# Kernel tuning notes

Hardware: AMD Instinct MI355X
Metric: run time of the kernel (lower is better)

The kernel has to match this reference:

```python
import jax, jax.numpy as jnp
import numpy as np

B, N, D, P = 4, 16384, 128, 100


def setup_inputs() -> dict:
    key = jax.random.key(0)
    k1, k2, k3 = jax.random.split(key, 3)
    x = jax.random.normal(k1, (B, N, D), dtype=jnp.float32)
    y = jax.random.normal(k2, (B, N, D), dtype=jnp.float32)
    thetas = jax.random.normal(k3, (P, D), dtype=jnp.float32)
    return {"x": x, "y": y, "thetas": thetas}


def reference(x, y, thetas):
    # Sliced OT (the branch taken since B*N*N*4 bytes >> memory limit).
    n_proj = thetas.shape[0]
    # F.normalize(theta, dim=0) per projection direction (eps clamp 1e-12)
    norms = jnp.maximum(jnp.linalg.norm(thetas, axis=-1, keepdims=True), 1e-12)
    thetas = thetas / norms  # (P, d)

    # Project all points onto all directions: (P, B, N)
    x_proj = jnp.einsum('bnd,pd->pbn', x, thetas)
    y_proj = jnp.einsum('bnd,pd->pbn', y, thetas)

    # torch: sort y_proj; scatter y_sorted back to original order of x via
    # x_indices = argsort(x_proj). Equivalent: transported_proj[n] =
    # y_sorted[rank_of_x_proj[n]], with rank = argsort(argsort(.)).
    y_sorted = jnp.sort(y_proj, axis=-1)
    ranks = jnp.argsort(jnp.argsort(x_proj, axis=-1), axis=-1)
    transported_proj = jnp.take_along_axis(y_sorted, ranks, axis=-1)  # (P, B, N)

    # Accumulate (transported_proj - x_proj) * theta over projections.
    transported = jnp.einsum('pbn,pd->bnd', transported_proj - x_proj, thetas)
    return x + transported / n_proj
```

## Files before the change

kernel.cpp:

```cpp
#include <hip/hip_runtime.h>
#include <hip/hip_bf16.h>

#define B_    4
#define N_    16384
#define D_    128
#define P_    100
#define BN_   65536
#define PBN_  6553600
#define PPAD  112
#define KPAD  128
#define NBIN  4096

typedef __attribute__((ext_vector_type(8))) short short8;
typedef __attribute__((ext_vector_type(4))) float floatx4;

__device__ __forceinline__ unsigned short f2b(float f) {
    unsigned u = __float_as_uint(f);
    return (unsigned short)((u + 0x7FFFu + ((u >> 16) & 1u)) >> 16);
}
__device__ __forceinline__ float b2f(unsigned short h) {
    return __uint_as_float(((unsigned)h) << 16);
}

__global__ void k_norm(const float* __restrict__ th,
                       unsigned short* __restrict__ thb,
                       unsigned short* __restrict__ thbT) {
    int p = blockIdx.x;
    int d = threadIdx.x;
    float v = 0.f;
    if (p < P_) v = th[p * D_ + d];
    float s = v * v;
    #pragma unroll
    for (int o = 32; o > 0; o >>= 1) s += __shfl_down(s, o, 64);
    __shared__ float red[2];
    if ((d & 63) == 0) red[d >> 6] = s;
    __syncthreads();
    float norm = fmaxf(sqrtf(red[0] + red[1]), 1e-12f);
    unsigned short r = f2b(v / norm);
    if (p < PPAD) thb[p * D_ + d] = r;
    thbT[d * KPAD + p] = r;
}

__global__ __launch_bounds__(256, 4) void k_proj(
    const float* __restrict__ x, const float* __restrict__ y,
    const unsigned short* __restrict__ thb,
    unsigned short* __restrict__ xp, unsigned short* __restrict__ yp) {
    __shared__ unsigned short th_s[15232];
    __shared__ unsigned short buf[8064];
    const int tid  = threadIdx.x;
    const int w    = tid >> 6;
    const int lane = tid & 63;
    const int n    = lane & 15;
    const int quad = lane >> 4;
    const int row0 = blockIdx.x * 64;

    for (int g = tid; g < 1792; g += 256) {
        int r = g >> 4, c = (g & 15) << 3;
        *(uint4*)(th_s + r * 136 + c) = *(const uint4*)(thb + r * D_ + c);
    }

    const float* xr = x + (size_t)(row0 + w * 16 + n) * D_ + quad * 8;
    const float* yr = y + (size_t)(row0 + w * 16 + n) * D_ + quad * 8;
    short8 bx[4], by[4];
    {
        float4 lx[8];
        #pragma unroll
        for (int ks = 0; ks < 4; ++ks) {
            lx[2*ks]   = *(const float4*)(xr + ks * 32);
            lx[2*ks+1] = *(const float4*)(xr + ks * 32 + 4);
        }
        #pragma unroll
        for (int ks = 0; ks < 4; ++ks) {
            short8 t;
            t[0] = (short)f2b(lx[2*ks].x);   t[1] = (short)f2b(lx[2*ks].y);
            t[2] = (short)f2b(lx[2*ks].z);   t[3] = (short)f2b(lx[2*ks].w);
            t[4] = (short)f2b(lx[2*ks+1].x); t[5] = (short)f2b(lx[2*ks+1].y);
            t[6] = (short)f2b(lx[2*ks+1].z); t[7] = (short)f2b(lx[2*ks+1].w);
            bx[ks] = t;
        }
    }
    {
        float4 ly[8];
        #pragma unroll
        for (int ks = 0; ks < 4; ++ks) {
            ly[2*ks]   = *(const float4*)(yr + ks * 32);
            ly[2*ks+1] = *(const float4*)(yr + ks * 32 + 4);
        }
        #pragma unroll
        for (int ks = 0; ks < 4; ++ks) {
            short8 t;
            t[0] = (short)f2b(ly[2*ks].x);   t[1] = (short)f2b(ly[2*ks].y);
            t[2] = (short)f2b(ly[2*ks].z);   t[3] = (short)f2b(ly[2*ks].w);
            t[4] = (short)f2b(ly[2*ks+1].x); t[5] = (short)f2b(ly[2*ks+1].y);
            t[6] = (short)f2b(ly[2*ks+1].z); t[7] = (short)f2b(ly[2*ks+1].w);
            by[ks] = t;
        }
    }
    __syncthreads();

    floatx4 ay[7];
    #pragma unroll
    for (int pt = 0; pt < 7; ++pt) {
        floatx4 accx = {0.f, 0.f, 0.f, 0.f};
        floatx4 accy = {0.f, 0.f, 0.f, 0.f};
        #pragma unroll
        for (int ks = 0; ks < 4; ++ks) {
            short8 a = *(const short8*)(th_s + (pt * 16 + n) * 136 + ks * 32 + quad * 8);
            accx = __builtin_amdgcn_mfma_f32_16x16x32_bf16(a, bx[ks], accx, 0, 0, 0);
            accy = __builtin_amdgcn_mfma_f32_16x16x32_bf16(a, by[ks], accy, 0, 0, 0);
        }
        #pragma unroll
        for (int reg = 0; reg < 4; ++reg)
            buf[(pt * 16 + quad * 4 + reg) * 72 + w * 16 + n] = f2b(accx[reg]);
        ay[pt] = accy;
    }
    __syncthreads();

    for (int g = tid; g < 800; g += 256) {
        int p = g >> 3, c = (g & 7) << 3;
        *(uint4*)(xp + (size_t)p * BN_ + row0 + c) = *(const uint4*)(buf + p * 72 + c);
    }
    __syncthreads();

    #pragma unroll
    for (int pt = 0; pt < 7; ++pt)
        #pragma unroll
        for (int reg = 0; reg < 4; ++reg)
            buf[(pt * 16 + quad * 4 + reg) * 72 + w * 16 + n] = f2b(ay[pt][reg]);
    __syncthreads();

    for (int g = tid; g < 800; g += 256) {
        int p = g >> 3, c = (g & 7) << 3;
        *(uint4*)(yp + (size_t)p * BN_ + row0 + c) = *(const uint4*)(buf + p * 72 + c);
    }
}

__device__ __forceinline__ int binof(float v) {
    int k = (int)((v + 8.0f) * 256.0f);
    return k < 0 ? 0 : (k > NBIN - 1 ? NBIN - 1 : k);
}

__device__ __forceinline__ void scan4(unsigned* hist, volatile unsigned* wsum, int t) {
    unsigned v[4], run = 0;
    #pragma unroll
    for (int i = 0; i < 4; ++i) { unsigned h = hist[t * 4 + i]; v[i] = run; run += h; }
    const int lane = t & 63, w = t >> 6;
    unsigned inc = run;
    #pragma unroll
    for (int off = 1; off < 64; off <<= 1) {
        unsigned nbr = __shfl_up(inc, off, 64);
        if (lane >= off) inc += nbr;
    }
    if (lane == 63) wsum[w] = inc;
    __syncthreads();
    if (t == 0) {
        unsigned r2 = 0;
        #pragma unroll
        for (int i = 0; i < 16; ++i) { unsigned h = wsum[i]; wsum[i] = r2; r2 += h; }
    }
    __syncthreads();
    unsigned base = wsum[w] + (inc - run);
    #pragma unroll
    for (int i = 0; i < 4; ++i) hist[t * 4 + i] = base + v[i];
}

__global__ __launch_bounds__(1024, 4) void k_sortdiff(
    const unsigned short* __restrict__ xp, const unsigned short* __restrict__ yp,
    unsigned short* __restrict__ diff) {
    __shared__ unsigned hist[NBIN];
    __shared__ unsigned short ysort[N_];
    __shared__ unsigned wsum[16];
    const int t = threadIdx.x;
    const unsigned* ypd = (const unsigned*)(yp + (size_t)blockIdx.x * N_);
    const unsigned* xpd = (const unsigned*)(xp + (size_t)blockIdx.x * N_);
    unsigned*       dfd = (unsigned*)(diff + (size_t)blockIdx.x * N_);

    unsigned yw[8], xw[8];
    #pragma unroll
    for (int i = 0; i < 2; ++i) {
        uint4 a = *(const uint4*)(ypd + i * 4096 + t * 4);
        yw[4*i] = a.x; yw[4*i+1] = a.y; yw[4*i+2] = a.z; yw[4*i+3] = a.w;
        uint4 c = *(const uint4*)(xpd + i * 4096 + t * 4);
        xw[4*i] = c.x; xw[4*i+1] = c.y; xw[4*i+2] = c.z; xw[4*i+3] = c.w;
    }

    #pragma unroll
    for (int i = 0; i < 4; ++i) hist[t + i * 1024] = 0;
    __syncthreads();

    unsigned jy[8], jx[8];
    #pragma unroll
    for (int k = 0; k < 8; ++k) {
        unsigned j0 = atomicAdd(&hist[binof(b2f((unsigned short)(yw[k] & 0xffff)))], 1u);
        unsigned j1 = atomicAdd(&hist[binof(b2f((unsigned short)(yw[k] >> 16)))], 1u);
        jy[k] = (j0 & 0xffffu) | (j1 << 16);
        unsigned i0 = atomicAdd(&hist[binof(b2f((unsigned short)(xw[k] & 0xffff)))], 0x10000u);
        unsigned i1 = atomicAdd(&hist[binof(b2f((unsigned short)(xw[k] >> 16)))], 0x10000u);
        jx[k] = (i0 >> 16) | (i1 & 0xffff0000u);
    }
    __syncthreads();
    scan4(hist, wsum, t);
    __syncthreads();

    #pragma unroll
    for (int k = 0; k < 8; ++k) {
        unsigned short e0 = (unsigned short)(yw[k] & 0xffff);
        unsigned short e1 = (unsigned short)(yw[k] >> 16);
        ysort[(hist[binof(b2f(e0))] & 0xffffu) + (jy[k] & 0xffffu)] = e0;
        ysort[(hist[binof(b2f(e1))] & 0xffffu) + (jy[k] >> 16)]     = e1;
        unsigned r0 = (hist[binof(b2f((unsigned short)(xw[k] & 0xffff)))] >> 16) + (jx[k] & 0xffffu);
        unsigned r1 = (hist[binof(b2f((unsigned short)(xw[k] >> 16)))] >> 16) + (jx[k] >> 16);
        jx[k] = r0 | (r1 << 16);
    }
    __syncthreads();

    #pragma unroll
    for (int i = 0; i < 2; ++i) {
        unsigned o[4];
        #pragma unroll
        for (int q = 0; q < 4; ++q) {
            int k = 4*i + q;
            float x0 = b2f((unsigned short)(xw[k] & 0xffff));
            float x1 = b2f((unsigned short)(xw[k] >> 16));
            unsigned short d0 = f2b(b2f(ysort[jx[k] & 0xffffu]) - x0);
            unsigned short d1 = f2b(b2f(ysort[jx[k] >> 16]) - x1);
            o[q] = (unsigned)d0 | ((unsigned)d1 << 16);
        }
        *(uint4*)(dfd + i * 4096 + t * 4) = make_uint4(o[0], o[1], o[2], o[3]);
    }
}

__global__ __launch_bounds__(256) void k_comb(
    const float* __restrict__ x, const unsigned short* __restrict__ diff,
    const unsigned short* __restrict__ thbT, float* __restrict__ out) {
    __shared__ unsigned short ths[128 * 136];
    __shared__ unsigned Lp[64 * 68];
    const int tid  = threadIdx.x;
    const int w    = tid >> 6;
    const int lane = tid & 63;
    const int n16  = lane & 15;
    const int quad = lane >> 4;
    const int row0 = blockIdx.x * 64;

    for (int g = tid; g < 2048; g += 256) {
        int r = g >> 4, c = (g & 15) << 3;
        *(uint4*)(ths + r * 136 + c) = *(const uint4*)(thbT + r * KPAD + c);
    }
    for (int g = tid; g < 952; g += 256) Lp[50 * 68 + g] = 0;
    for (int g = tid; g < 400; g += 256) {
        int p2 = g >> 3, rg = (g & 7) << 3;
        uint4 a = *(const uint4*)(diff + (size_t)(2 * p2) * BN_ + row0 + rg);
        uint4 b = *(const uint4*)(diff + (size_t)(2 * p2 + 1) * BN_ + row0 + rg);
        unsigned* dst = Lp + p2 * 68 + rg;
        dst[0] = (a.x & 0xffffu) | (b.x << 16);
        dst[1] = (a.x >> 16)     | (b.x & 0xffff0000u);
        dst[2] = (a.y & 0xffffu) | (b.y << 16);
        dst[3] = (a.y >> 16)     | (b.y & 0xffff0000u);
        dst[4] = (a.z & 0xffffu) | (b.z << 16);
        dst[5] = (a.z >> 16)     | (b.z & 0xffff0000u);
        dst[6] = (a.w & 0xffffu) | (b.w << 16);
        dst[7] = (a.w >> 16)     | (b.w & 0xffff0000u);
    }
    __syncthreads();

    const int r = w * 16 + n16;
    short8 af[4];
    #pragma unroll
    for (int ks = 0; ks < 4; ++ks) {
        union { unsigned u[4]; short8 v; } tu;
        #pragma unroll
        for (int m = 0; m < 4; ++m)
            tu.u[m] = Lp[(ks * 16 + quad * 4 + m) * 68 + r];
        af[ks] = tu.v;
    }

    floatx4 acc[8];
    #pragma unroll
    for (int nt = 0; nt < 8; ++nt) {
        acc[nt] = (floatx4){0.f, 0.f, 0.f, 0.f};
        #pragma unroll
        for (int ks = 0; ks < 4; ++ks) {
            short8 b = *(const short8*)(ths + (nt * 16 + n16) * 136 + ks * 32 + quad * 8);
            acc[nt] = __builtin_amdgcn_mfma_f32_16x16x32_bf16(af[ks], b, acc[nt], 0, 0, 0);
        }
    }

    const float invP = 1.0f / (float)P_;
    const size_t rbase = (size_t)(row0 + w * 16 + quad * 4) * D_ + n16;
    #pragma unroll
    for (int nt = 0; nt < 8; ++nt)
        #pragma unroll
        for (int reg = 0; reg < 4; ++reg) {
            size_t o = rbase + (size_t)reg * D_ + nt * 16;
            out[o] = fmaf(acc[nt][reg], invP, x[o]);
        }
}

extern "C" void kernel_launch(void* const* d_in, const int* in_sizes, int n_in,
                              void* d_out, int out_size, void* d_ws, size_t ws_size,
                              hipStream_t stream) {
    const float* x  = (const float*)d_in[0];
    const float* y  = (const float*)d_in[1];
    const float* th = (const float*)d_in[2];
    float* out = (float*)d_out;
    char*  wsb = (char*)d_ws;

    unsigned short* thb  = (unsigned short*)wsb;
    unsigned short* thbT = (unsigned short*)(wsb + 32768);
    unsigned short* xpb  = (unsigned short*)(wsb + 65536);
    unsigned short* ypb  = xpb + PBN_;

    k_norm<<<128, 128, 0, stream>>>(th, thb, thbT);
    k_proj<<<BN_ / 64, 256, 0, stream>>>(x, y, thb, xpb, ypb);
    k_sortdiff<<<P_ * B_, 1024, 0, stream>>>(xpb, ypb, xpb);
    k_comb<<<BN_ / 64, 256, 0, stream>>>(x, xpb, thbT, out);
}
```

Baseline: 144.2 us.

## Halve LDS staging buffers in projection and combine kernels to raise occupancy

The projection kernel now writes its x/y projection tiles in two passes (rows 0-63, then 64-111) through a smaller LDS buffer, so each block needs less shared memory. The combine kernel stages only half of the transposed theta matrix at a time, reloading the second half after the first half's output is written, and adds launch bounds of 4. The goal is more resident blocks per CU to hide memory latency, at the cost of extra barriers, a second theta load per block, and more serialized store phases.

After: 140.7 us. 1.03x faster.

```diff
diff --git a/kernel.cpp b/kernel.cpp
--- a/kernel.cpp
+++ b/kernel.cpp
@@ -46,7 +46,7 @@
     const unsigned short* __restrict__ thb,
     unsigned short* __restrict__ xp, unsigned short* __restrict__ yp) {
     __shared__ unsigned short th_s[15232];
-    __shared__ unsigned short buf[8064];
+    __shared__ unsigned short buf[4608];
     const int tid  = threadIdx.x;
     const int w    = tid >> 6;
     const int lane = tid & 63;
@@ -99,8 +99,9 @@
     __syncthreads();
 
     floatx4 ay[7];
-    #pragma unroll
-    for (int pt = 0; pt < 7; ++pt) {
+
+    #pragma unroll
+    for (int pt = 0; pt < 4; ++pt) {
         floatx4 accx = {0.f, 0.f, 0.f, 0.f};
         floatx4 accy = {0.f, 0.f, 0.f, 0.f};
         #pragma unroll
@@ -115,23 +116,55 @@
         ay[pt] = accy;
     }
     __syncthreads();
-
-    for (int g = tid; g < 800; g += 256) {
+    for (int g = tid; g < 512; g += 256) {
         int p = g >> 3, c = (g & 7) << 3;
         *(uint4*)(xp + (size_t)p * BN_ + row0 + c) = *(const uint4*)(buf + p * 72 + c);
     }
     __syncthreads();
 
     #pragma unroll
-    for (int pt = 0; pt < 7; ++pt)
+    for (int pt = 4; pt < 7; ++pt) {
+        floatx4 accx = {0.f, 0.f, 0.f, 0.f};
+        floatx4 accy = {0.f, 0.f, 0.f, 0.f};
+        #pragma unroll
+        for (int ks = 0; ks < 4; ++ks) {
+            short8 a = *(const short8*)(th_s + (pt * 16 + n) * 136 + ks * 32 + quad * 8);
+            accx = __builtin_amdgcn_mfma_f32_16x16x32_bf16(a, bx[ks], accx, 0, 0, 0);
+            accy = __builtin_amdgcn_mfma_f32_16x16x32_bf16(a, by[ks], accy, 0, 0, 0);
+        }
+        #pragma unroll
+        for (int reg = 0; reg < 4; ++reg)
+            buf[((pt - 4) * 16 + quad * 4 + reg) * 72 + w * 16 + n] = f2b(accx[reg]);
+        ay[pt] = accy;
+    }
+    __syncthreads();
+    for (int g = tid; g < 288; g += 256) {
+        int p = g >> 3, c = (g & 7) << 3;
+        *(uint4*)(xp + (size_t)(64 + p) * BN_ + row0 + c) = *(const uint4*)(buf + p * 72 + c);
+    }
+    __syncthreads();
+
+    #pragma unroll
+    for (int pt = 0; pt < 4; ++pt)
         #pragma unroll
         for (int reg = 0; reg < 4; ++reg)
             buf[(pt * 16 + quad * 4 + reg) * 72 + w * 16 + n] = f2b(ay[pt][reg]);
     __syncthreads();
-
-    for (int g = tid; g < 800; g += 256) {
+    for (int g = tid; g < 512; g += 256) {
         int p = g >> 3, c = (g & 7) << 3;
         *(uint4*)(yp + (size_t)p * BN_ + row0 + c) = *(const uint4*)(buf + p * 72 + c);
+    }
+    __syncthreads();
+
+    #pragma unroll
+    for (int pt = 4; pt < 7; ++pt)
+        #pragma unroll
+        for (int reg = 0; reg < 4; ++reg)
+            buf[((pt - 4) * 16 + quad * 4 + reg) * 72 + w * 16 + n] = f2b(ay[pt][reg]);
+    __syncthreads();
+    for (int g = tid; g < 288; g += 256) {
+        int p = g >> 3, c = (g & 7) << 3;
+        *(uint4*)(yp + (size_t)(64 + p) * BN_ + row0 + c) = *(const uint4*)(buf + p * 72 + c);
     }
 }
 
@@ -230,10 +263,10 @@
     }
 }
 
-__global__ __launch_bounds__(256) void k_comb(
+__global__ __launch_bounds__(256, 4) void k_comb(
     const float* __restrict__ x, const unsigned short* __restrict__ diff,
     const unsigned short* __restrict__ thbT, float* __restrict__ out) {
-    __shared__ unsigned short ths[128 * 136];
+    __shared__ unsigned short ths[64 * 136];
     __shared__ unsigned Lp[64 * 68];
     const int tid  = threadIdx.x;
     const int w    = tid >> 6;
@@ -242,7 +275,7 @@
     const int quad = lane >> 4;
     const int row0 = blockIdx.x * 64;
 
-    for (int g = tid; g < 2048; g += 256) {
+    for (int g = tid; g < 1024; g += 256) {
         int r = g >> 4, c = (g & 15) << 3;
         *(uint4*)(ths + r * 136 + c) = *(const uint4*)(thbT + r * KPAD + c);
     }
@@ -274,26 +307,45 @@
         af[ks] = tu.v;
     }
 
-    floatx4 acc[8];
-    #pragma unroll
-    for (int nt = 0; nt < 8; ++nt) {
-        acc[nt] = (floatx4){0.f, 0.f, 0.f, 0.f};
-        #pragma unroll
-        for (int ks = 0; ks < 4; ++ks) {
-            short8 b = *(const short8*)(ths + (nt * 16 + n16) * 136 + ks * 32 + quad * 8);
-            acc[nt] = __builtin_amdgcn_mfma_f32_16x16x32_bf16(af[ks], b, acc[nt], 0, 0, 0);
-        }
-    }
-
     const float invP = 1.0f / (float)P_;
     const size_t rbase = (size_t)(row0 + w * 16 + quad * 4) * D_ + n16;
-    #pragma unroll
-    for (int nt = 0; nt < 8; ++nt)
+
+    #pragma unroll
+    for (int nt = 0; nt < 4; ++nt) {
+        floatx4 acc = {0.f, 0.f, 0.f, 0.f};
+        #pragma unroll
+        for (int ks = 0; ks < 4; ++ks) {
+            short8 b = *(const short8*)(ths + (nt * 16 + n16) * 136 + ks * 32 + quad * 8);
+            acc = __builtin_amdgcn_mfma_f32_16x16x32_bf16(af[ks], b, acc, 0, 0, 0);
+        }
         #pragma unroll
         for (int reg = 0; reg < 4; ++reg) {
             size_t o = rbase + (size_t)reg * D_ + nt * 16;
-            out[o] = fmaf(acc[nt][reg], invP, x[o]);
-        }
+            out[o] = fmaf(acc[reg], invP, x[o]);
+        }
+    }
+    __syncthreads();
+
+    for (int g = tid; g < 1024; g += 256) {
+        int r2 = g >> 4, c = (g & 15) << 3;
+        *(uint4*)(ths + r2 * 136 + c) = *(const uint4*)(thbT + (size_t)(64 + r2) * KPAD + c);
+    }
+    __syncthreads();
+
+    #pragma unroll
+    for (int nt = 0; nt < 4; ++nt) {
+        floatx4 acc = {0.f, 0.f, 0.f, 0.f};
+        #pragma unroll
+        for (int ks = 0; ks < 4; ++ks) {
+            short8 b = *(const short8*)(ths + (nt * 16 + n16) * 136 + ks * 32 + quad * 8);
+            acc = __builtin_amdgcn_mfma_f32_16x16x32_bf16(af[ks], b, acc, 0, 0, 0);
+        }
+        #pragma unroll
+        for (int reg = 0; reg < 4; ++reg) {
+            size_t o = rbase + (size_t)reg * D_ + (64 + nt * 16);
+            out[o] = fmaf(acc[reg], invP, x[o]);
+        }
+    }
 }
 
 extern "C" void kernel_launch(void* const* d_in, const int* in_sizes, int n_in,
```
